# Performance work log

Hardware: AMD Instinct MI355X
Metric: run time of the kernel (lower is better)

The kernel has to match this reference:

```python
import jax, jax.numpy as jnp
import numpy as np

N = 50000      # nodes
E = 800000     # edges (avg degree 16)
D_IN = 128     # input_dim
H = 64         # hidden_dim (== output_dim)
L = 3          # num_layers


def setup_inputs() -> dict:
    key = jax.random.key(0)
    ks = jax.random.split(key, 24)
    s = 0.05
    p = lambda k, shape: jax.random.normal(k, shape, dtype=jnp.float32) * s
    inp = {}
    inp["node_features"] = jax.random.normal(ks[0], (N, D_IN), dtype=jnp.float32)
    inp["edge_index"] = jax.random.randint(ks[1], (2, E), 0, N, dtype=jnp.int32)
    # pre_mlp: Linear-ReLU-Linear (setup_LRL_nn with hidden_sizes=[hidden_dim])
    inp["pre_w1"] = p(ks[2], (D_IN, H)); inp["pre_b1"] = jnp.zeros((H,), jnp.float32)
    inp["pre_w2"] = p(ks[3], (H, H));    inp["pre_b2"] = jnp.zeros((H,), jnp.float32)
    # learnable skip gates (initialized to ones as in the module)
    inp["skip"] = jnp.ones((L, L), jnp.float32)
    # SAGEConv layers: lin_l (on mean-aggregated neighbors, with bias) + lin_r (root)
    for i in range(L):
        din = H * (i + 1)
        inp[f"wl{i}"] = p(ks[4 + 3 * i], (din, H))
        inp[f"bl{i}"] = jnp.zeros((H,), jnp.float32)
        inp[f"wr{i}"] = p(ks[5 + 3 * i], (din, H))
    # post_mlp: 256->64, 64->64, 64->256, 256->64
    inp["post_w1"] = p(ks[14], (H * (L + 1), H)); inp["post_b1"] = jnp.zeros((H,), jnp.float32)
    inp["post_w2"] = p(ks[15], (H, H));           inp["post_b2"] = jnp.zeros((H,), jnp.float32)
    inp["post_w3"] = p(ks[16], (H, 256));         inp["post_b3"] = jnp.zeros((256,), jnp.float32)
    inp["post_w4"] = p(ks[17], (256, H));         inp["post_b4"] = jnp.zeros((H,), jnp.float32)
    return inp


def _sage(x, src, dst, inv_deg, wl, bl, wr):
    # PyG SAGEConv (mean aggr): lin_l(mean_{j->i} x_j) + lin_r(x_i)
    agg = jax.ops.segment_sum(x[src], dst, num_segments=N) * inv_deg  # [N, Din]
    return agg @ wl + bl + x @ wr


def reference(node_features, edge_index,
              pre_w1, pre_b1, pre_w2, pre_b2, skip,
              wl0, bl0, wr0, wl1, bl1, wr1, wl2, bl2, wr2,
              post_w1, post_b1, post_w2, post_b2, post_w3, post_b3, post_w4, post_b4):
    src, dst = edge_index[0], edge_index[1]
    deg = jax.ops.segment_sum(jnp.ones((E,), jnp.float32), dst, num_segments=N)
    inv_deg = (1.0 / jnp.maximum(deg, 1.0))[:, None]  # [N,1]

    # pre_mlp
    x = jax.nn.relu(node_features @ pre_w1 + pre_b1) @ pre_w2 + pre_b2  # [N,H]

    layers = [(wl0, bl0, wr0), (wl1, bl1, wr1), (wl2, bl2, wr2)]
    all_emb = [x]
    emb = x
    for i, (wl, bl, wr) in enumerate(layers):
        gates = jax.nn.sigmoid(skip[i, :i + 1])  # [i+1]
        curr = jnp.concatenate([all_emb[j] * gates[j] for j in range(i + 1)], axis=1)  # [N, H*(i+1)]
        h = jax.nn.relu(_sage(curr, src, dst, inv_deg, wl, bl, wr))  # [N,H]  (dropout p=0)
        emb = jnp.concatenate([emb, h], axis=1)
        all_emb.append(h)

    s = jnp.sum(emb, axis=-2)  # sums over all nodes -> [H*(L+1)] (faithful to source)
    h = jax.nn.leaky_relu(s @ post_w1 + post_b1, negative_slope=0.1)
    h = jax.nn.relu(h @ post_w2 + post_b2)
    h = jax.nn.relu(h @ post_w3 + post_b3)
    return h @ post_w4 + post_b4  # [H]
```

## Files before the change

### kernel.cpp

```cpp
#include <hip/hip_runtime.h>
#include <math.h>

#define NN 50000
#define NE 800000
#define NB 196

typedef float v4f __attribute__((ext_vector_type(4)));
typedef float v2f __attribute__((ext_vector_type(2)));
typedef _Float16 v8h __attribute__((ext_vector_type(8)));

__device__ __forceinline__ unsigned char enc8(float v) {
#if __has_builtin(__builtin_amdgcn_cvt_pk_fp8_f32)
  return (unsigned char)(__builtin_amdgcn_cvt_pk_fp8_f32(v, v, 0, false) & 0xFF);
#else
  unsigned u = __float_as_uint(v);
  unsigned s = (u >> 24) & 0x80u;
  unsigned au = u & 0x7fffffffu;
  float a = __uint_as_float(au);
  if (au < 0x3C800000u) {
    int m = (int)(a * 512.0f + 0.5f);
    if (m >= 8) return (unsigned char)(s | 8u);
    return (unsigned char)(s | (unsigned)m);
  }
  unsigned r = au + 0x7FFFFu + ((au >> 20) & 1u);
  unsigned e = (r >> 23) - 120u;
  unsigned man = (r >> 20) & 7u;
  if (e > 15u) { e = 15u; man = 6u; }
  return (unsigned char)(s | (e << 3) | man);
#endif
}

#if __has_builtin(__builtin_amdgcn_cvt_pk_f32_fp8)
#define DEC8_HW 1
#else
__device__ __forceinline__ float dec8_1(unsigned b) {
  unsigned s = (b & 0x80u) << 24;
  unsigned em = b & 0x7fu;
  float v;
  if (em >= 8u) v = __uint_as_float((((em >> 3) + 120u) << 23) | ((em & 7u) << 20));
  else v = (float)em * 0.001953125f;
  return __uint_as_float(__float_as_uint(v) | s);
}
#endif

__device__ __forceinline__ void dec8x8(uint2 u, float* f) {
#ifdef DEC8_HW
  v2f p0 = __builtin_amdgcn_cvt_pk_f32_fp8((int)u.x, false);
  v2f p1 = __builtin_amdgcn_cvt_pk_f32_fp8((int)u.x, true);
  v2f p2 = __builtin_amdgcn_cvt_pk_f32_fp8((int)u.y, false);
  v2f p3 = __builtin_amdgcn_cvt_pk_f32_fp8((int)u.y, true);
  f[0] = p0.x; f[1] = p0.y; f[2] = p1.x; f[3] = p1.y;
  f[4] = p2.x; f[5] = p2.y; f[6] = p3.x; f[7] = p3.y;
#else
#pragma unroll
  for (int i = 0; i < 4; ++i) f[i] = dec8_1((u.x >> (8 * i)) & 0xFF);
#pragma unroll
  for (int i = 0; i < 4; ++i) f[4 + i] = dec8_1((u.y >> (8 * i)) & 0xFF);
#endif
}


__global__ __launch_bounds__(256) void k_bhist(const int* __restrict__ dst,
                                               int* __restrict__ gbcnt) {
  __shared__ int lcnt[NB];
  int t = threadIdx.x;
  for (int i = t; i < NB; i += 256) lcnt[i] = 0;
  __syncthreads();
  int eb = blockIdx.x * 4096;
#pragma unroll
  for (int i = 0; i < 16; ++i) {
    int e = eb + i * 256 + t;
    if (e < NE) atomicAdd(&lcnt[dst[e] >> 8], 1);
  }
  __syncthreads();
  for (int i = t; i < NB; i += 256)
    if (lcnt[i]) atomicAdd(&gbcnt[i], lcnt[i]);
}

__global__ __launch_bounds__(256) void k_bscan(const int* __restrict__ gbcnt,
                                               int* __restrict__ boff,
                                               int* __restrict__ gcur,
                                               int* __restrict__ offs,
                                               float* __restrict__ sv) {
  __shared__ int sd[256];
  int t = threadIdx.x;
  sv[t] = 0.f;
  int v = (t < NB) ? gbcnt[t] : 0;
  sd[t] = v;
  __syncthreads();
  for (int o = 1; o < 256; o <<= 1) {
    int u = (t >= o) ? sd[t - o] : 0;
    __syncthreads();
    sd[t] += u;
    __syncthreads();
  }
  if (t < NB) { int x = sd[t] - v; boff[t] = x; gcur[t] = x; }
  if (t == NB - 1) boff[NB] = sd[t];
  if (t == 0) offs[NN] = NE;
}

__global__ __launch_bounds__(256) void k_bscatter(const int* __restrict__ src,
                                                  const int* __restrict__ dst,
                                                  int* __restrict__ gcur,
                                                  unsigned* __restrict__ ebuf) {
  __shared__ int cnt[NB];
  __shared__ int base[NB];
  int t = threadIdx.x;
  for (int i = t; i < NB; i += 256) cnt[i] = 0;
  __syncthreads();
  int eb = blockIdx.x * 4096;
  unsigned pk[16];
  int bk[16], lp[16];
#pragma unroll
  for (int i = 0; i < 16; ++i) {
    int e = eb + i * 256 + t;
    if (e < NE) {
      int d = dst[e];
      int b = d >> 8;
      pk[i] = ((unsigned)src[e] << 8) | (unsigned)(d & 255);
      bk[i] = b;
      lp[i] = atomicAdd(&cnt[b], 1);
    }
  }
  __syncthreads();
  for (int i = t; i < NB; i += 256)
    base[i] = cnt[i] ? atomicAdd(&gcur[i], cnt[i]) : 0;
  __syncthreads();
#pragma unroll
  for (int i = 0; i < 16; ++i) {
    int e = eb + i * 256 + t;
    if (e < NE) ebuf[base[bk[i]] + lp[i]] = pk[i];
  }
}

__global__ __launch_bounds__(256) void k_bbuild(const unsigned* __restrict__ ebuf,
                                                const int* __restrict__ boff,
                                                int* __restrict__ offs,
                                                float* __restrict__ invd,
                                                int* __restrict__ csr) {
  __shared__ int dcnt[256];
  __shared__ int cur[256];
  int t = threadIdx.x;
  int b = blockIdx.x;
  int node0 = b << 8;
  int es = boff[b], ee = boff[b + 1];
  dcnt[t] = 0;
  __syncthreads();
  for (int e = es + t; e < ee; e += 256) atomicAdd(&dcnt[ebuf[e] & 255], 1);
  __syncthreads();
  int v = dcnt[t];
  cur[t] = v;
  __syncthreads();
  for (int o = 1; o < 256; o <<= 1) {
    int u = (t >= o) ? cur[t - o] : 0;
    __syncthreads();
    cur[t] += u;
    __syncthreads();
  }
  int excl = cur[t] - v;
  int node = node0 + t;
  if (node < NN) {
    offs[node] = es + excl;
    invd[node] = 1.0f / fmaxf((float)v, 1.0f);
  }
  __syncthreads();
  cur[t] = es + excl;
  __syncthreads();
  for (int e = es + t; e < ee; e += 256) {
    unsigned pk = ebuf[e];
    int p = atomicAdd(&cur[pk & 255], 1);
    csr[p] = (int)(pk >> 8);
  }
}

__global__ __launch_bounds__(256) void k_aggregate(
    const unsigned char* __restrict__ feat,
    const int* __restrict__ offs, const int* __restrict__ csr,
    const float* __restrict__ invd,
    _Float16* __restrict__ mean, int n) {
  int node = blockIdx.x * 4 + (threadIdx.x >> 6);
  int lane = threadIdx.x & 63;
  int slot = lane >> 3;
  int cg   = lane & 7;
  if (node >= n) return;
  int s = offs[node], e = offs[node + 1];

  float a[8];
#pragma unroll
  for (int i = 0; i < 8; ++i) a[i] = 0.f;

  if (e > s) {
    int emax = e - 1;
    for (int p0 = s; p0 < e; p0 += 16) {
      int pa = p0 + slot, pb = p0 + 8 + slot;
      int ja = __builtin_nontemporal_load(csr + (pa < emax ? pa : emax));
      int jb = __builtin_nontemporal_load(csr + (pb < emax ? pb : emax));
      uint2 ua = *(const uint2*)(feat + (size_t)ja * 64 + cg * 8);
      uint2 ub = *(const uint2*)(feat + (size_t)jb * 64 + cg * 8);
      float fa[8], fb[8];
      dec8x8(ua, fa);
      dec8x8(ub, fb);
      if (pa < e) {
#pragma unroll
        for (int i = 0; i < 8; ++i) a[i] += fa[i];
      }
      if (pb < e) {
#pragma unroll
        for (int i = 0; i < 8; ++i) a[i] += fb[i];
      }
    }
  }
#pragma unroll
  for (int i = 0; i < 8; ++i) {
    a[i] += __shfl_xor(a[i], 8, 64);
    a[i] += __shfl_xor(a[i], 16, 64);
    a[i] += __shfl_xor(a[i], 32, 64);
  }
  if (lane < 8) {
    float d = invd[node];
    v8h o;
#pragma unroll
    for (int i = 0; i < 8; ++i) o[i] = (_Float16)(a[i] * d);
    *(v8h*)(mean + (size_t)node * 64 + lane * 8) = o;
  }
}

struct LinArgs {
  const _Float16* a[6];
  const float* w[6];
  int gidx[6];
  int nsrc;
  const float* bias;
  const float* skip;
  _Float16* outp;
  unsigned char* out8;
  float* colsum;
  int n;
  int relu;
};

__global__ __launch_bounds__(256) void k_linear(LinArgs A) {
  __shared__ _Float16 sW[2][2][64 * 72];
  const int t    = threadIdx.x;
  const int lane = t & 63;
  const int wv   = t >> 6;
  const int qd   = lane >> 4;
  const int ln   = lane & 15;
  const int n0   = blockIdx.x * 64;

  v4f acc[4];
#pragma unroll
  for (int ct = 0; ct < 4; ++ct) acc[ct] = (v4f){0.f, 0.f, 0.f, 0.f};

  const int sn = t & 63;
  float wreg[16];
  auto loadW = [&](int s) {
    const float* w = A.w[s];
#pragma unroll
    for (int c = 0; c < 2; ++c) {
      int kb = (wv + 4 * c) * 8;
#pragma unroll
      for (int j = 0; j < 8; ++j)
        wreg[c * 8 + j] = w[(size_t)(kb + j) * 64 + sn];
    }
  };
  auto writeW = [&](int s, int b) {
    float gs = 1.0f;
    if (A.gidx[s] >= 0) gs = 1.0f / (1.0f + __expf(-A.skip[A.gidx[s]]));
#pragma unroll
    for (int c = 0; c < 2; ++c) {
      int cb = wv + 4 * c;
      v8h hv, lv;
#pragma unroll
      for (int j = 0; j < 8; ++j) {
        float f = wreg[c * 8 + j] * gs;
        _Float16 h = (_Float16)f;
        hv[j] = h;
        lv[j] = (_Float16)(f - (float)h);
      }
      *(v8h*)(&sW[b][0][sn * 72 + cb * 8]) = hv;
      *(v8h*)(&sW[b][1][sn * 72 + cb * 8]) = lv;
    }
  };

  const int arow = n0 + wv * 16 + ln;
  const bool arv = arow < A.n;
  v8h ah[2];
  auto loadA = [&](int s) {
    const _Float16* ph = A.a[s] + (size_t)arow * 64;
    if (arv) {
#pragma unroll
      for (int ks = 0; ks < 2; ++ks)
        ah[ks] = *(const v8h*)(ph + ks * 32 + qd * 8);
    } else {
      v8h z;
#pragma unroll
      for (int j = 0; j < 8; ++j) z[j] = (_Float16)0.f;
      ah[0] = ah[1] = z;
    }
  };

  loadW(0);
  writeW(0, 0);
  __syncthreads();

  for (int s = 0; s < A.nsrc; ++s) {
    loadA(s);
    if (s + 1 < A.nsrc) loadW(s + 1);
    const _Float16* wh = &sW[s & 1][0][0];
    const _Float16* wl = &sW[s & 1][1][0];
#pragma unroll
    for (int ks = 0; ks < 2; ++ks) {
#pragma unroll
      for (int ct = 0; ct < 4; ++ct) {
        int wn = ct * 16 + ln;
        v8h bh = *(const v8h*)(wh + wn * 72 + ks * 32 + qd * 8);
        v8h bl = *(const v8h*)(wl + wn * 72 + ks * 32 + qd * 8);
        acc[ct] = __builtin_amdgcn_mfma_f32_16x16x32_f16(ah[ks], bh, acc[ct], 0, 0, 0);
        acc[ct] = __builtin_amdgcn_mfma_f32_16x16x32_f16(ah[ks], bl, acc[ct], 0, 0, 0);
      }
    }
    if (s + 1 < A.nsrc) writeW(s + 1, (s + 1) & 1);
    __syncthreads();
  }

  float bvals[4];
#pragma unroll
  for (int ct = 0; ct < 4; ++ct) bvals[ct] = A.bias[ct * 16 + ln];

  unsigned char* f8t = (unsigned char*)&sW[1][0][0];
  float* red = (float*)&sW[0][0][0];

  float cs[4] = {0.f, 0.f, 0.f, 0.f};
#pragma unroll
  for (int ct = 0; ct < 4; ++ct) {
#pragma unroll
    for (int r = 0; r < 4; ++r) {
      int nb = wv * 16 + qd * 4 + r;
      int node = n0 + nb;
      float v = acc[ct][r] + bvals[ct];
      if (A.relu) v = fmaxf(v, 0.f);
      if (node < A.n) {
        if (A.outp) A.outp[(size_t)node * 64 + ct * 16 + ln] = (_Float16)v;
        if (A.out8) f8t[nb * 64 + ct * 16 + ln] = enc8(v);
        cs[ct] += v;
      }
    }
  }
  if (A.colsum) {
#pragma unroll
    for (int ct = 0; ct < 4; ++ct) {
      float v = cs[ct];
      v += __shfl_xor(v, 16, 64);
      v += __shfl_xor(v, 32, 64);
      if (qd == 0) red[wv * 64 + ct * 16 + ln] = v;
    }
  }
  if (A.out8 || A.colsum) __syncthreads();
  if (A.out8) {
    int row = t >> 2, ch = t & 3;
    if (n0 + row < A.n) {
      uint4 val = *(const uint4*)(f8t + row * 64 + ch * 16);
      *(uint4*)(A.out8 + (size_t)(n0 + row) * 64 + ch * 16) = val;
    }
  }
  if (A.colsum && t < 64) {
    float ssum = red[t] + red[64 + t] + red[128 + t] + red[192 + t];
    atomicAdd(&A.colsum[t], ssum);
  }
}

__global__ __launch_bounds__(256) void k_pre(
    const float* __restrict__ nf,
    const float* __restrict__ w1, const float* __restrict__ b1,
    const float* __restrict__ w2, const float* __restrict__ b2,
    _Float16* __restrict__ xout, unsigned char* __restrict__ x8,
    float* __restrict__ colsum, int n) {
  __shared__ _Float16 sW[2][2][64 * 72];
  __shared__ _Float16 atile[64 * 72];
  const int t    = threadIdx.x;
  const int lane = t & 63;
  const int wv   = t >> 6;
  const int qd   = lane >> 4;
  const int ln   = lane & 15;
  const int n0   = blockIdx.x * 64;
  const int sn   = t & 63;

  float wreg[16];
  auto loadW = [&](const float* w) {
#pragma unroll
    for (int c = 0; c < 2; ++c) {
      int kb = (wv + 4 * c) * 8;
#pragma unroll
      for (int j = 0; j < 8; ++j)
        wreg[c * 8 + j] = w[(size_t)(kb + j) * 64 + sn];
    }
  };
  auto writeW = [&](int b) {
#pragma unroll
    for (int c = 0; c < 2; ++c) {
      int cb = wv + 4 * c;
      v8h hv, lv;
#pragma unroll
      for (int j = 0; j < 8; ++j) {
        float f = wreg[c * 8 + j];
        _Float16 h = (_Float16)f;
        hv[j] = h;
        lv[j] = (_Float16)(f - (float)h);
      }
      *(v8h*)(&sW[b][0][sn * 72 + cb * 8]) = hv;
      *(v8h*)(&sW[b][1][sn * 72 + cb * 8]) = lv;
    }
  };

  const int arow = n0 + wv * 16 + ln;
  const bool arv = arow < n;
  v4f acc[4];
#pragma unroll
  for (int ct = 0; ct < 4; ++ct) acc[ct] = (v4f){0.f, 0.f, 0.f, 0.f};
  v8h ah[2];

  auto loadAf32 = [&](const float* base) {
#pragma unroll
    for (int ks = 0; ks < 2; ++ks) {
      v8h hv;
      if (arv) {
        const float* p = base + (size_t)arow * 128 + ks * 32 + qd * 8;
        float4 u0 = *(const float4*)(p);
        float4 u1 = *(const float4*)(p + 4);
        hv[0] = (_Float16)u0.x; hv[1] = (_Float16)u0.y;
        hv[2] = (_Float16)u0.z; hv[3] = (_Float16)u0.w;
        hv[4] = (_Float16)u1.x; hv[5] = (_Float16)u1.y;
        hv[6] = (_Float16)u1.z; hv[7] = (_Float16)u1.w;
      } else {
#pragma unroll
        for (int j = 0; j < 8; ++j) hv[j] = (_Float16)0.f;
      }
      ah[ks] = hv;
    }
  };
  auto domfma = [&](int b) {
    const _Float16* wh = &sW[b][0][0];
    const _Float16* wl = &sW[b][1][0];
#pragma unroll
    for (int ks = 0; ks < 2; ++ks) {
#pragma unroll
      for (int ct = 0; ct < 4; ++ct) {
        int wn = ct * 16 + ln;
        v8h bh = *(const v8h*)(wh + wn * 72 + ks * 32 + qd * 8);
        v8h bl = *(const v8h*)(wl + wn * 72 + ks * 32 + qd * 8);
        acc[ct] = __builtin_amdgcn_mfma_f32_16x16x32_f16(ah[ks], bh, acc[ct], 0, 0, 0);
        acc[ct] = __builtin_amdgcn_mfma_f32_16x16x32_f16(ah[ks], bl, acc[ct], 0, 0, 0);
      }
    }
  };

  loadW(w1);
  writeW(0);
  __syncthreads();
  loadAf32(nf);
  loadW(w1 + 64 * 64);
  domfma(0);
  writeW(1);
  __syncthreads();
  loadAf32(nf + 64);
  loadW(w2);
  domfma(1);
  writeW(0);

  float b1v[4];
#pragma unroll
  for (int ct = 0; ct < 4; ++ct) b1v[ct] = b1[ct * 16 + ln];
#pragma unroll
  for (int ct = 0; ct < 4; ++ct) {
#pragma unroll
    for (int r = 0; r < 4; ++r) {
      int nb = wv * 16 + qd * 4 + r;
      float v = fmaxf(acc[ct][r] + b1v[ct], 0.f);
      atile[nb * 72 + ct * 16 + ln] = (_Float16)v;
    }
  }
#pragma unroll
  for (int ct = 0; ct < 4; ++ct) acc[ct] = (v4f){0.f, 0.f, 0.f, 0.f};
  __syncthreads();

  const int trow = wv * 16 + ln;
#pragma unroll
  for (int ks = 0; ks < 2; ++ks)
    ah[ks] = *(const v8h*)(atile + trow * 72 + ks * 32 + qd * 8);
  domfma(0);

  float b2v[4];
#pragma unroll
  for (int ct = 0; ct < 4; ++ct) b2v[ct] = b2[ct * 16 + ln];

  unsigned char* f8t = (unsigned char*)&sW[1][0][0];
  float* red = (float*)&sW[0][0][0];
  float cs[4] = {0.f, 0.f, 0.f, 0.f};
  __syncthreads();
#pragma unroll
  for (int ct = 0; ct < 4; ++ct) {
#pragma unroll
    for (int r = 0; r < 4; ++r) {
      int nb = wv * 16 + qd * 4 + r;
      int node = n0 + nb;
      float v = acc[ct][r] + b2v[ct];
      if (node < n) {
        xout[(size_t)node * 64 + ct * 16 + ln] = (_Float16)v;
        f8t[nb * 64 + ct * 16 + ln] = enc8(v);
        cs[ct] += v;
      }
    }
  }
#pragma unroll
  for (int ct = 0; ct < 4; ++ct) {
    float v = cs[ct];
    v += __shfl_xor(v, 16, 64);
    v += __shfl_xor(v, 32, 64);
    if (qd == 0) red[wv * 64 + ct * 16 + ln] = v;
  }
  __syncthreads();
  {
    int row = t >> 2, ch = t & 3;
    if (n0 + row < n) {
      uint4 val = *(const uint4*)(f8t + row * 64 + ch * 16);
      *(uint4*)(x8 + (size_t)(n0 + row) * 64 + ch * 16) = val;
    }
  }
  if (t < 64) {
    float ssum = red[t] + red[64 + t] + red[128 + t] + red[192 + t];
    atomicAdd(&colsum[t], ssum);
  }
}

__global__ __launch_bounds__(256) void k_post(const float* __restrict__ s,
                                              const float* __restrict__ w1, const float* __restrict__ b1,
                                              const float* __restrict__ w2, const float* __restrict__ b2,
                                              const float* __restrict__ w3, const float* __restrict__ b3,
                                              const float* __restrict__ w4, const float* __restrict__ b4,
                                              float* __restrict__ outp) {
  __shared__ float sh[256], h1[64], h2[64], h3[256];
  int t = threadIdx.x;
  sh[t] = s[t];
  __syncthreads();
  if (t < 64) {
    float a = b1[t];
    for (int k = 0; k < 256; ++k) a += sh[k] * w1[k * 64 + t];
    h1[t] = (a >= 0.f) ? a : 0.1f * a;
  }
  __syncthreads();
  if (t < 64) {
    float a = b2[t];
    for (int k = 0; k < 64; ++k) a += h1[k] * w2[k * 64 + t];
    h2[t] = fmaxf(a, 0.f);
  }
  __syncthreads();
  {
    float a = b3[t];
    for (int k = 0; k < 64; ++k) a += h2[k] * w3[k * 256 + t];
    h3[t] = fmaxf(a, 0.f);
  }
  __syncthreads();
  if (t < 64) {
    float a = b4[t];
    for (int k = 0; k < 256; ++k) a += h3[k] * w4[k * 64 + t];
    outp[t] = a;
  }
}

extern "C" void kernel_launch(void* const* d_in, const int* in_sizes, int n_in,
                              void* d_out, int out_size, void* d_ws, size_t ws_size,
                              hipStream_t stream) {
  const float* nf     = (const float*)d_in[0];
  const int*   ei     = (const int*)d_in[1];
  const float* pre_w1 = (const float*)d_in[2];
  const float* pre_b1 = (const float*)d_in[3];
  const float* pre_w2 = (const float*)d_in[4];
  const float* pre_b2 = (const float*)d_in[5];
  const float* skip   = (const float*)d_in[6];
  const float* wl0 = (const float*)d_in[7],  *bl0 = (const float*)d_in[8],  *wr0 = (const float*)d_in[9];
  const float* wl1 = (const float*)d_in[10], *bl1 = (const float*)d_in[11], *wr1 = (const float*)d_in[12];
  const float* wl2 = (const float*)d_in[13], *bl2 = (const float*)d_in[14], *wr2 = (const float*)d_in[15];
  const float* pw1 = (const float*)d_in[16], *pb1 = (const float*)d_in[17];
  const float* pw2 = (const float*)d_in[18], *pb2 = (const float*)d_in[19];
  const float* pw3 = (const float*)d_in[20], *pb3 = (const float*)d_in[21];
  const float* pw4 = (const float*)d_in[22], *pb4 = (const float*)d_in[23];
  float* out = (float*)d_out;

  const int N = NN, E = NE;

  char* ws = (char*)d_ws;
  size_t pos = 0;
  auto alloc = [&](size_t bytes) {
    char* p = ws + pos;
    pos += (bytes + 255) & ~(size_t)255;
    return (void*)p;
  };
  int*      gbcnt = (int*)alloc((size_t)NB * 4);
  int*      boff  = (int*)alloc((size_t)(NB + 1) * 4);
  int*      gcur  = (int*)alloc((size_t)NB * 4);
  unsigned* ebuf  = (unsigned*)alloc((size_t)E * 4);
  int*      offs  = (int*)alloc((size_t)(N + 1) * 4);
  float*    invd  = (float*)alloc((size_t)N * 4);
  int*      csr   = (int*)alloc((size_t)E * 4);
  const size_t PB = (size_t)N * 64 * 2;
  _Float16* x  = (_Float16*)alloc(PB);
  _Float16* h0 = (_Float16*)alloc(PB);
  _Float16* h1 = (_Float16*)alloc(PB);
  _Float16* m0 = (_Float16*)alloc(PB);
  _Float16* m1 = (_Float16*)alloc(PB);
  _Float16* m2 = (_Float16*)alloc(PB);
  unsigned char* f8 = (unsigned char*)alloc((size_t)N * 64);
  float* sv = (float*)alloc(256 * 4);

  hipMemsetAsync(gbcnt, 0, (size_t)NB * 4, stream);

  const int* e_src = ei;
  const int* e_dst = ei + E;
  const int EGRID = (E + 4095) / 4096;
  k_bhist<<<EGRID, 256, 0, stream>>>(e_dst, gbcnt);
  k_bscan<<<1, 256, 0, stream>>>(gbcnt, boff, gcur, offs, sv);
  k_bscatter<<<EGRID, 256, 0, stream>>>(e_src, e_dst, gcur, ebuf);
  k_bbuild<<<NB, 256, 0, stream>>>(ebuf, boff, offs, invd, csr);

  const int LGRID = (N + 63) / 64;
  auto lin = [&](int nsrc,
                 const _Float16* a0, const float* w0, int g0,
                 const _Float16* a1, const float* w1_, int g1,
                 const _Float16* a2, const float* w2_, int g2,
                 const _Float16* a3, const float* w3_, int g3,
                 const _Float16* a4, const float* w4_, int g4,
                 const _Float16* a5, const float* w5_, int g5,
                 const float* bias, _Float16* op, unsigned char* o8,
                 float* colsum, int relu) {
    LinArgs A;
    A.a[0] = a0; A.a[1] = a1; A.a[2] = a2; A.a[3] = a3; A.a[4] = a4; A.a[5] = a5;
    A.w[0] = w0; A.w[1] = w1_; A.w[2] = w2_; A.w[3] = w3_; A.w[4] = w4_; A.w[5] = w5_;
    A.gidx[0] = g0; A.gidx[1] = g1; A.gidx[2] = g2; A.gidx[3] = g3; A.gidx[4] = g4; A.gidx[5] = g5;
    A.nsrc = nsrc; A.bias = bias; A.skip = skip;
    A.outp = op; A.out8 = o8; A.colsum = colsum;
    A.n = N; A.relu = relu;
    k_linear<<<LGRID, 256, 0, stream>>>(A);
  };

  k_pre<<<LGRID, 256, 0, stream>>>(nf, pre_w1, pre_b1, pre_w2, pre_b2,
                                   x, f8, sv, N);

  k_aggregate<<<(N + 3) / 4, 256, 0, stream>>>(f8, offs, csr, invd, m0, N);
  lin(2, m0, wl0, 0, x, wr0, 0,
      nullptr, nullptr, -1, nullptr, nullptr, -1,
      nullptr, nullptr, -1, nullptr, nullptr, -1,
      bl0, h0, f8, sv + 64, 1);

  k_aggregate<<<(N + 3) / 4, 256, 0, stream>>>(f8, offs, csr, invd, m1, N);
  lin(4, m0, wl1, 3, m1, wl1 + 64 * 64, 4,
      x, wr1, 3, h0, wr1 + 64 * 64, 4,
      nullptr, nullptr, -1, nullptr, nullptr, -1,
      bl1, h1, f8, sv + 128, 1);

  k_aggregate<<<(N + 3) / 4, 256, 0, stream>>>(f8, offs, csr, invd, m2, N);
  lin(6, m0, wl2, 6, m1, wl2 + 64 * 64, 7, m2, wl2 + 128 * 64, 8,
      x, wr2, 6, h0, wr2 + 64 * 64, 7, h1, wr2 + 128 * 64, 8,
      bl2, nullptr, nullptr, sv + 192, 1);

  k_post<<<1, 256, 0, stream>>>(sv, pw1, pb1, pw2, pb2, pw3, pb3, pw4, pb4, out);
}
```

Measured before the change: 356.6 us.

## Fuse neighbor mean aggregation into the SAGE linear kernel via shared-memory tile

Removes the separate k_aggregate launch and performs the CSR gather-mean inside k_linear. Each of four threads per node accumulates 16 FP8 channels, and the result goes into a shared-memory A tile that the MFMA loop reads directly. The mean is still written to global memory only when later layers need it, and the last layer's m2 buffer is dropped. This saves three launches and the mean write/read round trip. In exchange the gather uses a thread-per-node pattern with serial edge loops, which can cause load imbalance and lower occupancy because of the extra LDS tile and registers.

```diff
diff --git a/kernel.cpp b/kernel.cpp
--- a/kernel.cpp
+++ b/kernel.cpp
@@ -58,6 +58,10 @@
   for (int i = 0; i < 4; ++i) f[4 + i] = dec8_1((u.y >> (8 * i)) & 0xFF);
 #endif
 }
+__device__ __forceinline__ void dec8x16(uint4 u, float* f) {
+  dec8x8(make_uint2(u.x, u.y), f);
+  dec8x8(make_uint2(u.z, u.w), f + 8);
+}
 
 
 __global__ __launch_bounds__(256) void k_bhist(const int* __restrict__ dst,
@@ -173,63 +177,17 @@
   }
 }
 
-__global__ __launch_bounds__(256) void k_aggregate(
-    const unsigned char* __restrict__ feat,
-    const int* __restrict__ offs, const int* __restrict__ csr,
-    const float* __restrict__ invd,
-    _Float16* __restrict__ mean, int n) {
-  int node = blockIdx.x * 4 + (threadIdx.x >> 6);
-  int lane = threadIdx.x & 63;
-  int slot = lane >> 3;
-  int cg   = lane & 7;
-  if (node >= n) return;
-  int s = offs[node], e = offs[node + 1];
-
-  float a[8];
-#pragma unroll
-  for (int i = 0; i < 8; ++i) a[i] = 0.f;
-
-  if (e > s) {
-    int emax = e - 1;
-    for (int p0 = s; p0 < e; p0 += 16) {
-      int pa = p0 + slot, pb = p0 + 8 + slot;
-      int ja = __builtin_nontemporal_load(csr + (pa < emax ? pa : emax));
-      int jb = __builtin_nontemporal_load(csr + (pb < emax ? pb : emax));
-      uint2 ua = *(const uint2*)(feat + (size_t)ja * 64 + cg * 8);
-      uint2 ub = *(const uint2*)(feat + (size_t)jb * 64 + cg * 8);
-      float fa[8], fb[8];
-      dec8x8(ua, fa);
-      dec8x8(ub, fb);
-      if (pa < e) {
-#pragma unroll
-        for (int i = 0; i < 8; ++i) a[i] += fa[i];
-      }
-      if (pb < e) {
-#pragma unroll
-        for (int i = 0; i < 8; ++i) a[i] += fb[i];
-      }
-    }
-  }
-#pragma unroll
-  for (int i = 0; i < 8; ++i) {
-    a[i] += __shfl_xor(a[i], 8, 64);
-    a[i] += __shfl_xor(a[i], 16, 64);
-    a[i] += __shfl_xor(a[i], 32, 64);
-  }
-  if (lane < 8) {
-    float d = invd[node];
-    v8h o;
-#pragma unroll
-    for (int i = 0; i < 8; ++i) o[i] = (_Float16)(a[i] * d);
-    *(v8h*)(mean + (size_t)node * 64 + lane * 8) = o;
-  }
-}
-
 struct LinArgs {
   const _Float16* a[6];
   const float* w[6];
   int gidx[6];
   int nsrc;
+  int fusedsrc;
+  const unsigned char* feat8;
+  const int* offs;
+  const int* csr;
+  const float* invd;
+  _Float16* mout;
   const float* bias;
   const float* skip;
   _Float16* outp;
@@ -241,6 +199,7 @@
 
 __global__ __launch_bounds__(256) void k_linear(LinArgs A) {
   __shared__ _Float16 sW[2][2][64 * 72];
+  __shared__ _Float16 atile[64 * 72];
   const int t    = threadIdx.x;
   const int lane = t & 63;
   const int wv   = t >> 6;
@@ -248,10 +207,6 @@
   const int ln   = lane & 15;
   const int n0   = blockIdx.x * 64;
 
-  v4f acc[4];
-#pragma unroll
-  for (int ct = 0; ct < 4; ++ct) acc[ct] = (v4f){0.f, 0.f, 0.f, 0.f};
-
   const int sn = t & 63;
   float wreg[16];
   auto loadW = [&](int s) {
@@ -283,12 +238,75 @@
     }
   };
 
+  loadW(0);
+
+  if (A.fusedsrc >= 0) {
+    const int nd = t >> 2;
+    const int q  = t & 3;
+    const int node = n0 + nd;
+    float a[16];
+#pragma unroll
+    for (int i = 0; i < 16; ++i) a[i] = 0.f;
+    float dinv = 0.f;
+    if (node < A.n) {
+      int s = A.offs[node], e = A.offs[node + 1];
+      dinv = A.invd[node];
+      const unsigned char* fb = A.feat8;
+      int p = s;
+      for (; p + 4 <= e; p += 4) {
+        int j0 = __builtin_nontemporal_load(A.csr + p);
+        int j1 = __builtin_nontemporal_load(A.csr + p + 1);
+        int j2 = __builtin_nontemporal_load(A.csr + p + 2);
+        int j3 = __builtin_nontemporal_load(A.csr + p + 3);
+        uint4 u0 = *(const uint4*)(fb + (size_t)j0 * 64 + q * 16);
+        uint4 u1 = *(const uint4*)(fb + (size_t)j1 * 64 + q * 16);
+        uint4 u2 = *(const uint4*)(fb + (size_t)j2 * 64 + q * 16);
+        uint4 u3 = *(const uint4*)(fb + (size_t)j3 * 64 + q * 16);
+        float f0[16], f1[16], f2[16], f3[16];
+        dec8x16(u0, f0); dec8x16(u1, f1); dec8x16(u2, f2); dec8x16(u3, f3);
+#pragma unroll
+        for (int i = 0; i < 16; ++i) a[i] += (f0[i] + f1[i]) + (f2[i] + f3[i]);
+      }
+      for (; p < e; ++p) {
+        int j = __builtin_nontemporal_load(A.csr + p);
+        uint4 u = *(const uint4*)(fb + (size_t)j * 64 + q * 16);
+        float f[16];
+        dec8x16(u, f);
+#pragma unroll
+        for (int i = 0; i < 16; ++i) a[i] += f[i];
+      }
+    }
+    v8h o0, o1;
+#pragma unroll
+    for (int i = 0; i < 8; ++i) {
+      o0[i] = (_Float16)(a[i] * dinv);
+      o1[i] = (_Float16)(a[8 + i] * dinv);
+    }
+    *(v8h*)(&atile[nd * 72 + q * 16]) = o0;
+    *(v8h*)(&atile[nd * 72 + q * 16 + 8]) = o1;
+    if (A.mout && node < A.n) {
+      *(v8h*)(A.mout + (size_t)node * 64 + q * 16) = o0;
+      *(v8h*)(A.mout + (size_t)node * 64 + q * 16 + 8) = o1;
+    }
+  }
+
+  writeW(0, 0);
+  __syncthreads();
+
+  v4f acc[4];
+#pragma unroll
+  for (int ct = 0; ct < 4; ++ct) acc[ct] = (v4f){0.f, 0.f, 0.f, 0.f};
+
   const int arow = n0 + wv * 16 + ln;
   const bool arv = arow < A.n;
   v8h ah[2];
   auto loadA = [&](int s) {
-    const _Float16* ph = A.a[s] + (size_t)arow * 64;
-    if (arv) {
+    if (s == A.fusedsrc) {
+      const _Float16* ph = atile + (wv * 16 + ln) * 72;
+      ah[0] = *(const v8h*)(ph + qd * 8);
+      ah[1] = *(const v8h*)(ph + 32 + qd * 8);
+    } else if (arv) {
+      const _Float16* ph = A.a[s] + (size_t)arow * 64;
 #pragma unroll
       for (int ks = 0; ks < 2; ++ks)
         ah[ks] = *(const v8h*)(ph + ks * 32 + qd * 8);
@@ -299,10 +317,6 @@
       ah[0] = ah[1] = z;
     }
   };
-
-  loadW(0);
-  writeW(0, 0);
-  __syncthreads();
 
   for (int s = 0; s < A.nsrc; ++s) {
     loadA(s);
@@ -609,7 +623,6 @@
   _Float16* h1 = (_Float16*)alloc(PB);
   _Float16* m0 = (_Float16*)alloc(PB);
   _Float16* m1 = (_Float16*)alloc(PB);
-  _Float16* m2 = (_Float16*)alloc(PB);
   unsigned char* f8 = (unsigned char*)alloc((size_t)N * 64);
   float* sv = (float*)alloc(256 * 4);
 
@@ -624,7 +637,7 @@
   k_bbuild<<<NB, 256, 0, stream>>>(ebuf, boff, offs, invd, csr);
 
   const int LGRID = (N + 63) / 64;
-  auto lin = [&](int nsrc,
+  auto lin = [&](int nsrc, int fusedsrc, _Float16* mout,
                  const _Float16* a0, const float* w0, int g0,
                  const _Float16* a1, const float* w1_, int g1,
                  const _Float16* a2, const float* w2_, int g2,
@@ -637,7 +650,10 @@
     A.a[0] = a0; A.a[1] = a1; A.a[2] = a2; A.a[3] = a3; A.a[4] = a4; A.a[5] = a5;
     A.w[0] = w0; A.w[1] = w1_; A.w[2] = w2_; A.w[3] = w3_; A.w[4] = w4_; A.w[5] = w5_;
     A.gidx[0] = g0; A.gidx[1] = g1; A.gidx[2] = g2; A.gidx[3] = g3; A.gidx[4] = g4; A.gidx[5] = g5;
-    A.nsrc = nsrc; A.bias = bias; A.skip = skip;
+    A.nsrc = nsrc; A.fusedsrc = fusedsrc;
+    A.feat8 = f8; A.offs = offs; A.csr = csr; A.invd = invd;
+    A.mout = mout;
+    A.bias = bias; A.skip = skip;
     A.outp = op; A.out8 = o8; A.colsum = colsum;
     A.n = N; A.relu = relu;
     k_linear<<<LGRID, 256, 0, stream>>>(A);
@@ -646,20 +662,20 @@
   k_pre<<<LGRID, 256, 0, stream>>>(nf, pre_w1, pre_b1, pre_w2, pre_b2,
                                    x, f8, sv, N);
 
-  k_aggregate<<<(N + 3) / 4, 256, 0, stream>>>(f8, offs, csr, invd, m0, N);
-  lin(2, m0, wl0, 0, x, wr0, 0,
+  lin(2, 0, m0,
+      nullptr, wl0, 0, x, wr0, 0,
       nullptr, nullptr, -1, nullptr, nullptr, -1,
       nullptr, nullptr, -1, nullptr, nullptr, -1,
       bl0, h0, f8, sv + 64, 1);
 
-  k_aggregate<<<(N + 3) / 4, 256, 0, stream>>>(f8, offs, csr, invd, m1, N);
-  lin(4, m0, wl1, 3, m1, wl1 + 64 * 64, 4,
+  lin(4, 1, m1,
+      m0, wl1, 3, nullptr, wl1 + 64 * 64, 4,
       x, wr1, 3, h0, wr1 + 64 * 64, 4,
       nullptr, nullptr, -1, nullptr, nullptr, -1,
       bl1, h1, f8, sv + 128, 1);
 
-  k_aggregate<<<(N + 3) / 4, 256, 0, stream>>>(f8, offs, csr, invd, m2, N);
-  lin(6, m0, wl2, 6, m1, wl2 + 64 * 64, 7, m2, wl2 + 128 * 64, 8,
+  lin(6, 2, nullptr,
+      m0, wl2, 6, m1, wl2 + 64 * 64, 7, nullptr, wl2 + 128 * 64, 8,
       x, wr2, 6, h0, wr2 + 64 * 64, 7, h1, wr2 + 128 * 64, 8,
       bl2, nullptr, nullptr, sv + 192, 1);
 
```

New measurement: 333.2 us. 6.6% less time.
